# Optimization experiments

Hardware: AMD Instinct MI355X
Metric: run time of the kernel (lower is better)

The kernel has to match this reference:

```python
import jax, jax.numpy as jnp
import numpy as np

TOP_K = 2


def setup_inputs() -> dict:
    key = jax.random.key(0)
    k1, k2, k3, k4, k5 = jax.random.split(key, 5)
    B, S, H, F, E = 4, 2048, 1024, 4096, 8
    scale = 1.0 / np.sqrt(H)
    return {
        "hidden_states": jax.random.normal(k1, (B, S, H), dtype=jnp.float32),
        "gate_w": jax.random.normal(k2, (E, H), dtype=jnp.float32) * scale,
        "w1": jax.random.normal(k3, (E, F, H), dtype=jnp.float32) * scale,
        "w3": jax.random.normal(k4, (E, F, H), dtype=jnp.float32) * scale,
        "w2": jax.random.normal(k5, (E, H, F), dtype=jnp.float32) * (1.0 / np.sqrt(F)),
    }


def reference(hidden_states, gate_w, w1, w3, w2):
    B, S, H = hidden_states.shape
    E = gate_w.shape[0]
    x = hidden_states.reshape(-1, H)                    # [T, H], T = B*S

    router_logits = x @ gate_w.T                        # [T, E]
    probs = jax.nn.softmax(router_logits.astype(jnp.float32), axis=-1)
    top_w, top_i = jax.lax.top_k(probs, TOP_K)          # [T, k]
    top_w = top_w / jnp.sum(top_w, axis=-1, keepdims=True)
    top_w = top_w.astype(x.dtype)

    # combine weight of each expert for each token: [E, T]
    one_hot = jax.nn.one_hot(top_i, E, dtype=x.dtype)   # [T, k, E]
    comb = jnp.einsum("tke,tk->et", one_hot, top_w)

    # loop over experts via scan; tokens not routed to expert e have comb==0,
    # which matches the gather/FFN/scatter-combine of the original exactly.
    def body(acc, wts):
        w1e, w3e, w2e, ce = wts
        h = jax.nn.silu(x @ w1e.T) * (x @ w3e.T)        # [T, F]
        return acc + (h @ w2e.T) * ce[:, None], None

    out0 = jnp.zeros_like(x)
    out, _ = jax.lax.scan(body, out0, (w1, w3, w2, comb))
    return out.reshape(B, S, H), router_logits
```

## Files before the change

### kernel.cpp

```cpp
#include <hip/hip_runtime.h>
#include <hip/hip_bf16.h>

#define T_TOK 8192
#define HDIM  1024
#define FDIM  4096
#define NEXP  8

typedef __attribute__((ext_vector_type(8))) short short8;
typedef __attribute__((ext_vector_type(4))) float f32x4;
typedef unsigned short u16;
typedef unsigned int   u32;

#define XB_OFF    0ull
#define W1B_OFF   (XB_OFF   + 16777216ull)
#define W3B_OFF   (W1B_OFF  + 67108864ull)
#define W2B_OFF   (W3B_OFF  + 67108864ull)
#define HBUF_OFF  (W2B_OFF  + 67108864ull)
#define CNT_OFF   (HBUF_OFF + 134217728ull)
#define HOFF_OFF  (CNT_OFF  + 64ull)
#define TLIST_OFF (HOFF_OFF + 64ull)
#define WLIST_OFF (TLIST_OFF + 262144ull)
#define WS_NEED   (WLIST_OFF + 262144ull)

__device__ __forceinline__ u16 f2bf(float f) {
  u32 u = __float_as_uint(f);
  return (u16)((u + 0x7fffu + ((u >> 16) & 1u)) >> 16);
}

__device__ __forceinline__ void gl_lds16(const void* g, void* l) {
  __builtin_amdgcn_global_load_lds(
      (const __attribute__((address_space(1))) void*)g,
      (__attribute__((address_space(3))) void*)l, 16, 0, 0);
}

__global__ __launch_bounds__(256) void convert_kernel(const float* __restrict__ src,
                                                      u16* __restrict__ dst, int n4) {
  int stride = gridDim.x * blockDim.x;
  for (int i = blockIdx.x * blockDim.x + threadIdx.x; i < n4; i += stride) {
    float4 v = ((const float4*)src)[i];
    u32 lo = (u32)f2bf(v.x) | ((u32)f2bf(v.y) << 16);
    u32 hi = (u32)f2bf(v.z) | ((u32)f2bf(v.w) << 16);
    ((uint2*)dst)[i] = make_uint2(lo, hi);
  }
}

__global__ __launch_bounds__(256) void router_kernel(
    const float* __restrict__ x, const float* __restrict__ gw,
    float* __restrict__ logits, u16* __restrict__ xb,
    int* __restrict__ counts, int* __restrict__ tlist, float* __restrict__ wlist) {
  const int wid = threadIdx.x >> 6, lane = threadIdx.x & 63;
  const int t = blockIdx.x * 4 + wid;
  const float* xr = x + (size_t)t * HDIM + lane * 16;
  float4 xv[4];
#pragma unroll
  for (int q = 0; q < 4; ++q) xv[q] = ((const float4*)xr)[q];

  u32 pk[8];
#pragma unroll
  for (int q = 0; q < 4; ++q) {
    pk[q * 2 + 0] = (u32)f2bf(xv[q].x) | ((u32)f2bf(xv[q].y) << 16);
    pk[q * 2 + 1] = (u32)f2bf(xv[q].z) | ((u32)f2bf(xv[q].w) << 16);
  }
  u32* xbo = (u32*)(xb + (size_t)t * HDIM + lane * 16);
  ((uint4*)xbo)[0] = make_uint4(pk[0], pk[1], pk[2], pk[3]);
  ((uint4*)xbo)[1] = make_uint4(pk[4], pk[5], pk[6], pk[7]);

  float lg[NEXP];
#pragma unroll
  for (int e = 0; e < NEXP; ++e) {
    const float4* g = (const float4*)(gw + (size_t)e * HDIM + lane * 16);
    float s = 0.f;
#pragma unroll
    for (int q = 0; q < 4; ++q) {
      float4 gv = g[q];
      s += xv[q].x * gv.x + xv[q].y * gv.y + xv[q].z * gv.z + xv[q].w * gv.w;
    }
#pragma unroll
    for (int off = 32; off > 0; off >>= 1) s += __shfl_xor(s, off, 64);
    lg[e] = s;
  }
  if (lane == 0) {
    float* lo = logits + (size_t)t * NEXP;
#pragma unroll
    for (int e = 0; e < NEXP; ++e) lo[e] = lg[e];
    float v1 = -1e30f, v2 = -1e30f; int i1 = 0, i2 = 0;
#pragma unroll
    for (int e = 0; e < NEXP; ++e) {
      float le = lg[e];
      if (le > v1)      { v2 = v1; i2 = i1; v1 = le; i1 = e; }
      else if (le > v2) { v2 = le; i2 = e; }
    }
    float t2 = __expf(v2 - v1);
    float rs = 1.f / (1.f + t2);
    int p1 = atomicAdd(&counts[i1], 1);
    tlist[i1 * T_TOK + p1] = t; wlist[i1 * T_TOK + p1] = rs;
    int p2 = atomicAdd(&counts[i2], 1);
    tlist[i2 * T_TOK + p2] = t; wlist[i2 * T_TOK + p2] = t2 * rs;
  }
}

__global__ void prefix_kernel(const int* __restrict__ counts, int* __restrict__ hoff) {
  if (threadIdx.x == 0) {
    int s = 0;
    for (int e = 0; e < NEXP; ++e) { hoff[e] = s; s += counts[e]; }
    hoff[NEXP] = s;
  }
}

__global__ __launch_bounds__(256, 2) void ffn1_kernel(
    const u16* __restrict__ xb, const u16* __restrict__ w1b, const u16* __restrict__ w3b,
    u16* __restrict__ hbuf, const int* __restrict__ counts, const int* __restrict__ hoff,
    const int* __restrict__ tlist) {
  const int bid = blockIdx.x;
  const int e  = bid & 7;
  const int j  = bid >> 3;
  const int ct = j >> 6;
  const int rt = j & 63;
  const int Ne = counts[e];
  if (rt * 128 >= Ne) return;

  __shared__ u16 Alds[128 * 64];
  __shared__ u16 B1lds[128 * 64];
  __shared__ u16 B3lds[128 * 64];

  const int tid = threadIdx.x;
  const int wid = tid >> 6, lane = tid & 63;
  const int wr = wid >> 1, wc = wid & 1;
  const int lr = lane & 15, lhi = lane >> 4;

  size_t aoff[4], boff[4]; int ldso[4];
#pragma unroll
  for (int q = 0; q < 4; ++q) {
    int i = wid * 4 + q;
    int r = i * 8 + (lane >> 3);
    int sw = ((lane & 7) ^ (r & 7)) * 8;
    int grow = rt * 128 + r;
    int gi = grow < Ne ? grow : Ne - 1;
    int tok = tlist[e * T_TOK + gi];
    aoff[q] = (size_t)tok * HDIM + sw;
    int fr = ct * 128 + r;
    boff[q] = ((size_t)e * FDIM + fr) * HDIM + sw;
    ldso[q] = i * 512;
  }

  f32x4 acc1[4][4] = {}; f32x4 acc3[4][4] = {};

  for (int k0 = 0; k0 < HDIM; k0 += 64) {
    __syncthreads();
#pragma unroll
    for (int q = 0; q < 4; ++q) {
      gl_lds16(xb  + aoff[q] + k0, Alds  + ldso[q]);
      gl_lds16(w1b + boff[q] + k0, B1lds + ldso[q]);
      gl_lds16(w3b + boff[q] + k0, B3lds + ldso[q]);
    }
    __syncthreads();
#pragma unroll
    for (int kk = 0; kk < 2; ++kk) {
      const int swo = ((kk * 4 + lhi) ^ (lr & 7)) * 8;
      short8 af[4], b1f[4], b3f[4];
#pragma unroll
      for (int m = 0; m < 4; ++m)
        af[m] = *(const short8*)(Alds + (wr * 64 + m * 16 + lr) * 64 + swo);
#pragma unroll
      for (int n = 0; n < 4; ++n) {
        int o = (wc * 64 + n * 16 + lr) * 64 + swo;
        b1f[n] = *(const short8*)(B1lds + o);
        b3f[n] = *(const short8*)(B3lds + o);
      }
#pragma unroll
      for (int m = 0; m < 4; ++m)
#pragma unroll
        for (int n = 0; n < 4; ++n) {
          acc1[m][n] = __builtin_amdgcn_mfma_f32_16x16x32_bf16(af[m], b1f[n], acc1[m][n], 0, 0, 0);
          acc3[m][n] = __builtin_amdgcn_mfma_f32_16x16x32_bf16(af[m], b3f[n], acc3[m][n], 0, 0, 0);
        }
    }
  }

  const int hb = hoff[e];
  const int rbase = rt * 128 + wr * 64 + lhi * 4;
  const int cbase = ct * 128 + wc * 64 + lr;
#pragma unroll
  for (int m = 0; m < 4; ++m)
#pragma unroll
    for (int i = 0; i < 4; ++i) {
      int grow = rbase + m * 16 + i;
      if (grow < Ne) {
        size_t rowp = (size_t)(hb + grow) * FDIM + cbase;
#pragma unroll
        for (int n = 0; n < 4; ++n) {
          float a1 = acc1[m][n][i], a3 = acc3[m][n][i];
          float hv = (a1 / (1.f + __expf(-a1))) * a3;
          hbuf[rowp + n * 16] = f2bf(hv);
        }
      }
    }
}

__global__ __launch_bounds__(256, 2) void ffn2_kernel(
    const u16* __restrict__ hbuf, const u16* __restrict__ w2b,
    float* __restrict__ out, const int* __restrict__ counts, const int* __restrict__ hoff,
    const int* __restrict__ tlist, const float* __restrict__ wlist) {
  const int bid = blockIdx.x;
  const int e  = bid & 7;
  const int j  = bid >> 3;
  const int ct = j >> 6;
  const int rt = j & 63;
  const int Ne = counts[e];
  if (rt * 128 >= Ne) return;
  const int hb = hoff[e];

  __shared__ u16 Alds[128 * 64];
  __shared__ u16 Blds[128 * 64];

  const int tid = threadIdx.x;
  const int wid = tid >> 6, lane = tid & 63;
  const int wr = wid >> 1, wc = wid & 1;
  const int lr = lane & 15, lhi = lane >> 4;

  size_t aoff[4], boff[4]; int ldso[4];
#pragma unroll
  for (int q = 0; q < 4; ++q) {
    int i = wid * 4 + q;
    int r = i * 8 + (lane >> 3);
    int sw = ((lane & 7) ^ (r & 7)) * 8;
    int grow = rt * 128 + r;
    int gi = grow < Ne ? grow : Ne - 1;
    aoff[q] = (size_t)(hb + gi) * FDIM + sw;
    int hr = ct * 128 + r;
    boff[q] = ((size_t)e * HDIM + hr) * FDIM + sw;
    ldso[q] = i * 512;
  }

  f32x4 acc[4][4] = {};

  for (int k0 = 0; k0 < FDIM; k0 += 64) {
    __syncthreads();
#pragma unroll
    for (int q = 0; q < 4; ++q) {
      gl_lds16(hbuf + aoff[q] + k0, Alds + ldso[q]);
      gl_lds16(w2b + boff[q] + k0, Blds + ldso[q]);
    }
    __syncthreads();
#pragma unroll
    for (int kk = 0; kk < 2; ++kk) {
      const int swo = ((kk * 4 + lhi) ^ (lr & 7)) * 8;
      short8 af[4], bf_[4];
#pragma unroll
      for (int m = 0; m < 4; ++m)
        af[m] = *(const short8*)(Alds + (wr * 64 + m * 16 + lr) * 64 + swo);
#pragma unroll
      for (int n = 0; n < 4; ++n)
        bf_[n] = *(const short8*)(Blds + (wc * 64 + n * 16 + lr) * 64 + swo);
#pragma unroll
      for (int m = 0; m < 4; ++m)
#pragma unroll
        for (int n = 0; n < 4; ++n)
          acc[m][n] = __builtin_amdgcn_mfma_f32_16x16x32_bf16(af[m], bf_[n], acc[m][n], 0, 0, 0);
    }
  }

  const int rb = rt * 128 + wr * 64 + lhi * 4;
  const int cb = ct * 128 + wc * 64 + lr;
#pragma unroll
  for (int m = 0; m < 4; ++m)
#pragma unroll
    for (int i = 0; i < 4; ++i) {
      int grow = rb + m * 16 + i;
      if (grow < Ne) {
        int tok = tlist[e * T_TOK + grow];
        float wt = wlist[e * T_TOK + grow];
        float* op = out + (size_t)tok * HDIM + cb;
#pragma unroll
        for (int n = 0; n < 4; ++n)
          atomicAdd(op + n * 16, wt * acc[m][n][i]);
      }
    }
}

extern "C" void kernel_launch(void* const* d_in, const int* in_sizes, int n_in,
                              void* d_out, int out_size, void* d_ws, size_t ws_size,
                              hipStream_t stream) {
  (void)in_sizes; (void)n_in; (void)out_size;
  if (ws_size < WS_NEED) return;

  const float* x  = (const float*)d_in[0];
  const float* gw = (const float*)d_in[1];
  const float* w1 = (const float*)d_in[2];
  const float* w3 = (const float*)d_in[3];
  const float* w2 = (const float*)d_in[4];
  float* out = (float*)d_out;
  float* logits = out + (size_t)T_TOK * HDIM;

  char* ws = (char*)d_ws;
  u16* xb    = (u16*)(ws + XB_OFF);
  u16* w1b   = (u16*)(ws + W1B_OFF);
  u16* w3b   = (u16*)(ws + W3B_OFF);
  u16* w2b   = (u16*)(ws + W2B_OFF);
  u16* hbuf  = (u16*)(ws + HBUF_OFF);
  int* counts = (int*)(ws + CNT_OFF);
  int* hoffp  = (int*)(ws + HOFF_OFF);
  int* tlist  = (int*)(ws + TLIST_OFF);
  float* wlist = (float*)(ws + WLIST_OFF);

  hipMemsetAsync(d_out, 0, (size_t)T_TOK * HDIM * sizeof(float), stream);
  hipMemsetAsync(counts, 0, NEXP * sizeof(int), stream);

  const int n4 = NEXP * FDIM * HDIM / 4;
  convert_kernel<<<4096, 256, 0, stream>>>(w1, w1b, n4);
  convert_kernel<<<4096, 256, 0, stream>>>(w3, w3b, n4);
  convert_kernel<<<4096, 256, 0, stream>>>(w2, w2b, n4);
  router_kernel<<<T_TOK / 4, 256, 0, stream>>>(x, gw, logits, xb, counts, tlist, wlist);
  prefix_kernel<<<1, 64, 0, stream>>>(counts, hoffp);
  ffn1_kernel<<<NEXP * 64 * 32, 256, 0, stream>>>(xb, w1b, w3b, hbuf, counts, hoffp, tlist);
  ffn2_kernel<<<NEXP * 64 * 8, 256, 0, stream>>>(hbuf, w2b, out, counts, hoffp, tlist, wlist);
}
```

Before: 865.7 us.

## Enlarge MoE GEMM tiles to 256 rows, prefetch next K-stage, fuse weight conversions

New measurement: 989.2 us. 14.3% more time.

```diff
diff --git a/kernel.cpp b/kernel.cpp
--- a/kernel.cpp
+++ b/kernel.cpp
@@ -33,14 +33,21 @@
       (__attribute__((address_space(3))) void*)l, 16, 0, 0);
 }
 
-__global__ __launch_bounds__(256) void convert_kernel(const float* __restrict__ src,
-                                                      u16* __restrict__ dst, int n4) {
+__global__ __launch_bounds__(256) void convert3_kernel(
+    const float* __restrict__ s0, const float* __restrict__ s1, const float* __restrict__ s2,
+    u16* __restrict__ d0, u16* __restrict__ d1, u16* __restrict__ d2) {
+  const int n4 = NEXP * FDIM * HDIM / 4;
+  const int total = 3 * n4;
   int stride = gridDim.x * blockDim.x;
-  for (int i = blockIdx.x * blockDim.x + threadIdx.x; i < n4; i += stride) {
-    float4 v = ((const float4*)src)[i];
+  for (int i = blockIdx.x * blockDim.x + threadIdx.x; i < total; i += stride) {
+    int seg = i >> 23;
+    int j = i & (n4 - 1);
+    const float* s = seg == 0 ? s0 : (seg == 1 ? s1 : s2);
+    u16* d = seg == 0 ? d0 : (seg == 1 ? d1 : d2);
+    float4 v = ((const float4*)s)[j];
     u32 lo = (u32)f2bf(v.x) | ((u32)f2bf(v.y) << 16);
     u32 hi = (u32)f2bf(v.z) | ((u32)f2bf(v.w) << 16);
-    ((uint2*)dst)[i] = make_uint2(lo, hi);
+    ((uint2*)d)[j] = make_uint2(lo, hi);
   }
 }
 
@@ -107,19 +114,19 @@
   }
 }
 
-__global__ __launch_bounds__(256, 2) void ffn1_kernel(
+__global__ __launch_bounds__(512, 1) void ffn1_kernel(
     const u16* __restrict__ xb, const u16* __restrict__ w1b, const u16* __restrict__ w3b,
     u16* __restrict__ hbuf, const int* __restrict__ counts, const int* __restrict__ hoff,
     const int* __restrict__ tlist) {
   const int bid = blockIdx.x;
   const int e  = bid & 7;
   const int j  = bid >> 3;
-  const int ct = j >> 6;
-  const int rt = j & 63;
+  const int ct = j >> 5;
+  const int rt = j & 31;
   const int Ne = counts[e];
-  if (rt * 128 >= Ne) return;
-
-  __shared__ u16 Alds[128 * 64];
+  if (rt * 256 >= Ne) return;
+
+  __shared__ u16 Alds[256 * 64];
   __shared__ u16 B1lds[128 * 64];
   __shared__ u16 B3lds[128 * 64];
 
@@ -128,57 +135,69 @@
   const int wr = wid >> 1, wc = wid & 1;
   const int lr = lane & 15, lhi = lane >> 4;
 
-  size_t aoff[4], boff[4]; int ldso[4];
-#pragma unroll
-  for (int q = 0; q < 4; ++q) {
-    int i = wid * 4 + q;
-    int r = i * 8 + (lane >> 3);
-    int sw = ((lane & 7) ^ (r & 7)) * 8;
-    int grow = rt * 128 + r;
+  const int swcol = ((lane & 7) ^ ((lane >> 3) & 7)) * 8;
+  const int rowl  = tid >> 3;
+
+  size_t aoff[4]; int ldsoA[4];
+#pragma unroll
+  for (int i = 0; i < 4; ++i) {
+    int grow = rt * 256 + i * 64 + rowl;
     int gi = grow < Ne ? grow : Ne - 1;
     int tok = tlist[e * T_TOK + gi];
-    aoff[q] = (size_t)tok * HDIM + sw;
-    int fr = ct * 128 + r;
-    boff[q] = ((size_t)e * FDIM + fr) * HDIM + sw;
-    ldso[q] = i * 512;
-  }
+    aoff[i] = (size_t)tok * HDIM + swcol;
+    ldsoA[i] = (i * 64 + wid * 8) * 64;
+  }
+  size_t b1off[2], b3off[2]; int ldsoB[2];
+#pragma unroll
+  for (int i = 0; i < 2; ++i) {
+    int fr = ct * 128 + i * 64 + rowl;
+    b1off[i] = ((size_t)e * FDIM + fr) * HDIM + swcol;
+    b3off[i] = b1off[i];
+    ldsoB[i] = (i * 64 + wid * 8) * 64;
+  }
+
+#define FFN1_STAGE(K0) do { \
+  _Pragma("unroll") for (int i_ = 0; i_ < 4; ++i_) gl_lds16(xb  + aoff[i_]  + (K0), Alds  + ldsoA[i_]); \
+  _Pragma("unroll") for (int i_ = 0; i_ < 2; ++i_) gl_lds16(w1b + b1off[i_] + (K0), B1lds + ldsoB[i_]); \
+  _Pragma("unroll") for (int i_ = 0; i_ < 2; ++i_) gl_lds16(w3b + b3off[i_] + (K0), B3lds + ldsoB[i_]); \
+} while (0)
 
   f32x4 acc1[4][4] = {}; f32x4 acc3[4][4] = {};
+  FFN1_STAGE(0);
 
   for (int k0 = 0; k0 < HDIM; k0 += 64) {
     __syncthreads();
-#pragma unroll
-    for (int q = 0; q < 4; ++q) {
-      gl_lds16(xb  + aoff[q] + k0, Alds  + ldso[q]);
-      gl_lds16(w1b + boff[q] + k0, B1lds + ldso[q]);
-      gl_lds16(w3b + boff[q] + k0, B3lds + ldso[q]);
-    }
-    __syncthreads();
+    short8 af[2][4], b1f[2][4], b3f[2][4];
 #pragma unroll
     for (int kk = 0; kk < 2; ++kk) {
       const int swo = ((kk * 4 + lhi) ^ (lr & 7)) * 8;
-      short8 af[4], b1f[4], b3f[4];
 #pragma unroll
       for (int m = 0; m < 4; ++m)
-        af[m] = *(const short8*)(Alds + (wr * 64 + m * 16 + lr) * 64 + swo);
+        af[kk][m] = *(const short8*)(Alds + (wr * 64 + m * 16 + lr) * 64 + swo);
 #pragma unroll
       for (int n = 0; n < 4; ++n) {
         int o = (wc * 64 + n * 16 + lr) * 64 + swo;
-        b1f[n] = *(const short8*)(B1lds + o);
-        b3f[n] = *(const short8*)(B3lds + o);
+        b1f[kk][n] = *(const short8*)(B1lds + o);
+        b3f[kk][n] = *(const short8*)(B3lds + o);
       }
+    }
+    __syncthreads();
+    if (k0 + 64 < HDIM) FFN1_STAGE(k0 + 64);
+    __builtin_amdgcn_s_setprio(1);
+#pragma unroll
+    for (int kk = 0; kk < 2; ++kk)
 #pragma unroll
       for (int m = 0; m < 4; ++m)
 #pragma unroll
         for (int n = 0; n < 4; ++n) {
-          acc1[m][n] = __builtin_amdgcn_mfma_f32_16x16x32_bf16(af[m], b1f[n], acc1[m][n], 0, 0, 0);
-          acc3[m][n] = __builtin_amdgcn_mfma_f32_16x16x32_bf16(af[m], b3f[n], acc3[m][n], 0, 0, 0);
+          acc1[m][n] = __builtin_amdgcn_mfma_f32_16x16x32_bf16(af[kk][m], b1f[kk][n], acc1[m][n], 0, 0, 0);
+          acc3[m][n] = __builtin_amdgcn_mfma_f32_16x16x32_bf16(af[kk][m], b3f[kk][n], acc3[m][n], 0, 0, 0);
         }
-    }
+    __builtin_amdgcn_s_setprio(0);
   }
 
   const int hb = hoff[e];
-  const int rbase = rt * 128 + wr * 64 + lhi * 4;
+  const int rbase = rt * 256 + wr * 64 + lhi * 4;
   const int cbase = ct * 128 + wc * 64 + lr;
 #pragma unroll
   for (int m = 0; m < 4; ++m)
@@ -195,22 +214,23 @@
         }
       }
     }
-}
-
-__global__ __launch_bounds__(256, 2) void ffn2_kernel(
+#undef FFN1_STAGE
+}
+
+__global__ __launch_bounds__(512, 1) void ffn2_kernel(
     const u16* __restrict__ hbuf, const u16* __restrict__ w2b,
     float* __restrict__ out, const int* __restrict__ counts, const int* __restrict__ hoff,
     const int* __restrict__ tlist, const float* __restrict__ wlist) {
   const int bid = blockIdx.x;
   const int e  = bid & 7;
   const int j  = bid >> 3;
-  const int ct = j >> 6;
-  const int rt = j & 63;
+  const int ct = j >> 5;
+  const int rt = j & 31;
   const int Ne = counts[e];
-  if (rt * 128 >= Ne) return;
+  if (rt * 256 >= Ne) return;
   const int hb = hoff[e];
 
-  __shared__ u16 Alds[128 * 64];
+  __shared__ u16 Alds[256 * 64];
   __shared__ u16 Blds[128 * 64];
 
   const int tid = threadIdx.x;
@@ -218,49 +238,60 @@
   const int wr = wid >> 1, wc = wid & 1;
   const int lr = lane & 15, lhi = lane >> 4;
 
-  size_t aoff[4], boff[4]; int ldso[4];
-#pragma unroll
-  for (int q = 0; q < 4; ++q) {
-    int i = wid * 4 + q;
-    int r = i * 8 + (lane >> 3);
-    int sw = ((lane & 7) ^ (r & 7)) * 8;
-    int grow = rt * 128 + r;
+  const int swcol = ((lane & 7) ^ ((lane >> 3) & 7)) * 8;
+  const int rowl  = tid >> 3;
+
+  size_t aoff[4]; int ldsoA[4];
+#pragma unroll
+  for (int i = 0; i < 4; ++i) {
+    int grow = rt * 256 + i * 64 + rowl;
     int gi = grow < Ne ? grow : Ne - 1;
-    aoff[q] = (size_t)(hb + gi) * FDIM + sw;
-    int hr = ct * 128 + r;
-    boff[q] = ((size_t)e * HDIM + hr) * FDIM + sw;
-    ldso[q] = i * 512;
-  }
+    aoff[i] = (size_t)(hb + gi) * FDIM + swcol;
+    ldsoA[i] = (i * 64 + wid * 8) * 64;
+  }
+  size_t boff[2]; int ldsoB[2];
+#pragma unroll
+  for (int i = 0; i < 2; ++i) {
+    int hr = ct * 128 + i * 64 + rowl;
+    boff[i] = ((size_t)e * HDIM + hr) * FDIM + swcol;
+    ldsoB[i] = (i * 64 + wid * 8) * 64;
+  }
+
+#define FFN2_STAGE(K0) do { \
+  _Pragma("unroll") for (int i_ = 0; i_ < 4; ++i_) gl_lds16(hbuf + aoff[i_] + (K0), Alds + ldsoA[i_]); \
+  _Pragma("unroll") for (int i_ = 0; i_ < 2; ++i_) gl_lds16(w2b  + boff[i_] + (K0), Blds + ldsoB[i_]); \
+} while (0)
 
   f32x4 acc[4][4] = {};
+  FFN2_STAGE(0);
 
   for (int k0 = 0; k0 < FDIM; k0 += 64) {
     __syncthreads();
-#pragma unroll
-    for (int q = 0; q < 4; ++q) {
-      gl_lds16(hbuf + aoff[q] + k0, Alds + ldso[q]);
-      gl_lds16(w2b + boff[q] + k0, Blds + ldso[q]);
-    }
-    __syncthreads();
+    short8 af[2][4], bf_[2][4];
 #pragma unroll
     for (int kk = 0; kk < 2; ++kk) {
       const int swo = ((kk * 4 + lhi) ^ (lr & 7)) * 8;
-      short8 af[4], bf_[4];
 #pragma unroll
       for (int m = 0; m < 4; ++m)
-        af[m] = *(const short8*)(Alds + (wr * 64 + m * 16 + lr) * 64 + swo);
+        af[kk][m] = *(const short8*)(Alds + (wr * 64 + m * 16 + lr) * 64 + swo);
 #pragma unroll
       for (int n = 0; n < 4; ++n)
-        bf_[n] = *(const short8*)(Blds + (wc * 64 + n * 16 + lr) * 64 + swo);
+        bf_[kk][n] = *(const short8*)(Blds + (wc * 64 + n * 16 + lr) * 64 + swo);
+    }
+    __syncthreads();
+    if (k0 + 64 < FDIM) FFN2_STAGE(k0 + 64);
+    __builtin_amdgcn_s_setprio(1);
+#pragma unroll
+    for (int kk = 0; kk < 2; ++kk)
 #pragma unroll
       for (int m = 0; m < 4; ++m)
 #pragma unroll
         for (int n = 0; n < 4; ++n)
-          acc[m][n] = __builtin_amdgcn_mfma_f32_16x16x32_bf16(af[m], bf_[n], acc[m][n], 0, 0, 0);
-    }
-  }
-
-  const int rb = rt * 128 + wr * 64 + lhi * 4;
+          acc[m][n] = __builtin_amdgcn_mfma_f32_16x16x32_bf16(af[kk][m], bf_[kk][n], acc[m][n], 0, 0, 0);
+    __builtin_amdgcn_s_setprio(0);
+  }
+
+  const int rb = rt * 256 + wr * 64 + lhi * 4;
   const int cb = ct * 128 + wc * 64 + lr;
 #pragma unroll
   for (int m = 0; m < 4; ++m)
@@ -276,6 +307,7 @@
           atomicAdd(op + n * 16, wt * acc[m][n][i]);
       }
     }
+#undef FFN2_STAGE
 }
 
 extern "C" void kernel_launch(void* const* d_in, const int* in_sizes, int n_in,
@@ -306,12 +338,9 @@
   hipMemsetAsync(d_out, 0, (size_t)T_TOK * HDIM * sizeof(float), stream);
   hipMemsetAsync(counts, 0, NEXP * sizeof(int), stream);
 
-  const int n4 = NEXP * FDIM * HDIM / 4;
-  convert_kernel<<<4096, 256, 0, stream>>>(w1, w1b, n4);
-  convert_kernel<<<4096, 256, 0, stream>>>(w3, w3b, n4);
-  convert_kernel<<<4096, 256, 0, stream>>>(w2, w2b, n4);
+  convert3_kernel<<<8192, 256, 0, stream>>>(w1, w3, w2, w1b, w3b, w2b);
   router_kernel<<<T_TOK / 4, 256, 0, stream>>>(x, gw, logits, xb, counts, tlist, wlist);
   prefix_kernel<<<1, 64, 0, stream>>>(counts, hoffp);
-  ffn1_kernel<<<NEXP * 64 * 32, 256, 0, stream>>>(xb, w1b, w3b, hbuf, counts, hoffp, tlist);
-  ffn2_kernel<<<NEXP * 64 * 8, 256, 0, stream>>>(hbuf, w2b, out, counts, hoffp, tlist, wlist);
-}
+  ffn1_kernel<<<NEXP * 32 * 32, 512, 0, stream>>>(xb, w1b, w3b, hbuf, counts, hoffp, tlist);
+  ffn2_kernel<<<NEXP * 8 * 32, 512, 0, stream>>>(hbuf, w2b, out, counts, hoffp, tlist, wlist);
+}
```

## Fuse weight conversion with router and use 8-wave ffn1 blocks

Applied to the files above, without the earlier changes.

Measured after the change: 833.2 us. -3.8%, faster.

```diff
diff --git a/kernel.cpp b/kernel.cpp
--- a/kernel.cpp
+++ b/kernel.cpp
@@ -33,23 +33,34 @@
       (__attribute__((address_space(3))) void*)l, 16, 0, 0);
 }
 
-__global__ __launch_bounds__(256) void convert_kernel(const float* __restrict__ src,
-                                                      u16* __restrict__ dst, int n4) {
-  int stride = gridDim.x * blockDim.x;
-  for (int i = blockIdx.x * blockDim.x + threadIdx.x; i < n4; i += stride) {
-    float4 v = ((const float4*)src)[i];
-    u32 lo = (u32)f2bf(v.x) | ((u32)f2bf(v.y) << 16);
-    u32 hi = (u32)f2bf(v.z) | ((u32)f2bf(v.w) << 16);
-    ((uint2*)dst)[i] = make_uint2(lo, hi);
-  }
-}
-
-__global__ __launch_bounds__(256) void router_kernel(
+__global__ __launch_bounds__(256) void prep_kernel(
     const float* __restrict__ x, const float* __restrict__ gw,
+    const float* __restrict__ s0, const float* __restrict__ s1, const float* __restrict__ s2,
+    u16* __restrict__ d0, u16* __restrict__ d1, u16* __restrict__ d2,
     float* __restrict__ logits, u16* __restrict__ xb,
     int* __restrict__ counts, int* __restrict__ tlist, float* __restrict__ wlist) {
+  if (blockIdx.x < 8192) {
+    const int n8 = NEXP * FDIM * HDIM / 8;
+    const int total = 3 * n8;
+    const int stride = 8192 * 256;
+    for (int i = blockIdx.x * 256 + threadIdx.x; i < total; i += stride) {
+      int seg = i >> 22;
+      int j = i & (n8 - 1);
+      const float* s = seg == 0 ? s0 : (seg == 1 ? s1 : s2);
+      u16* d = seg == 0 ? d0 : (seg == 1 ? d1 : d2);
+      float4 v0 = ((const float4*)s)[j * 2];
+      float4 v1 = ((const float4*)s)[j * 2 + 1];
+      uint4 o;
+      o.x = (u32)f2bf(v0.x) | ((u32)f2bf(v0.y) << 16);
+      o.y = (u32)f2bf(v0.z) | ((u32)f2bf(v0.w) << 16);
+      o.z = (u32)f2bf(v1.x) | ((u32)f2bf(v1.y) << 16);
+      o.w = (u32)f2bf(v1.z) | ((u32)f2bf(v1.w) << 16);
+      ((uint4*)d)[j] = o;
+    }
+    return;
+  }
   const int wid = threadIdx.x >> 6, lane = threadIdx.x & 63;
-  const int t = blockIdx.x * 4 + wid;
+  const int t = (blockIdx.x - 8192) * 4 + wid;
   const float* xr = x + (size_t)t * HDIM + lane * 16;
   float4 xv[4];
 #pragma unroll
@@ -107,7 +118,7 @@
   }
 }
 
-__global__ __launch_bounds__(256, 2) void ffn1_kernel(
+__global__ __launch_bounds__(512, 2) void ffn1_kernel(
     const u16* __restrict__ xb, const u16* __restrict__ w1b, const u16* __restrict__ w3b,
     u16* __restrict__ hbuf, const int* __restrict__ counts, const int* __restrict__ hoff,
     const int* __restrict__ tlist) {
@@ -119,58 +130,56 @@
   const int Ne = counts[e];
   if (rt * 128 >= Ne) return;
 
-  __shared__ u16 Alds[128 * 64];
-  __shared__ u16 B1lds[128 * 64];
-  __shared__ u16 B3lds[128 * 64];
+  __shared__ u16 LDS[24576];
 
   const int tid = threadIdx.x;
   const int wid = tid >> 6, lane = tid & 63;
-  const int wr = wid >> 1, wc = wid & 1;
+  const int wr = wid >> 2, wc = wid & 3;
   const int lr = lane & 15, lhi = lane >> 4;
 
-  size_t aoff[4], boff[4]; int ldso[4];
-#pragma unroll
-  for (int q = 0; q < 4; ++q) {
-    int i = wid * 4 + q;
-    int r = i * 8 + (lane >> 3);
-    int sw = ((lane & 7) ^ (r & 7)) * 8;
+  size_t aoff[2], b1off[2], b3off[2];
+#pragma unroll
+  for (int q = 0; q < 2; ++q) {
+    int idx = q * 512 + tid;
+    int r = idx >> 3, c = idx & 7;
+    int sw = (c ^ (r & 7)) * 8;
     int grow = rt * 128 + r;
     int gi = grow < Ne ? grow : Ne - 1;
-    int tok = tlist[e * T_TOK + gi];
-    aoff[q] = (size_t)tok * HDIM + sw;
+    aoff[q]  = (size_t)tlist[e * T_TOK + gi] * HDIM + sw;
     int fr = ct * 128 + r;
-    boff[q] = ((size_t)e * FDIM + fr) * HDIM + sw;
-    ldso[q] = i * 512;
-  }
-
-  f32x4 acc1[4][4] = {}; f32x4 acc3[4][4] = {};
+    b1off[q] = ((size_t)e * FDIM + fr) * HDIM + sw;
+    b3off[q] = b1off[q];
+  }
+  const int dW = wid * 512;
+
+  f32x4 acc1[4][2] = {}, acc3[4][2] = {};
 
   for (int k0 = 0; k0 < HDIM; k0 += 64) {
     __syncthreads();
 #pragma unroll
-    for (int q = 0; q < 4; ++q) {
-      gl_lds16(xb  + aoff[q] + k0, Alds  + ldso[q]);
-      gl_lds16(w1b + boff[q] + k0, B1lds + ldso[q]);
-      gl_lds16(w3b + boff[q] + k0, B3lds + ldso[q]);
+    for (int q = 0; q < 2; ++q) {
+      gl_lds16(xb  + aoff[q]  + k0, LDS + q * 4096 + dW);
+      gl_lds16(w1b + b1off[q] + k0, LDS + 8192 + q * 4096 + dW);
+      gl_lds16(w3b + b3off[q] + k0, LDS + 16384 + q * 4096 + dW);
     }
     __syncthreads();
 #pragma unroll
     for (int kk = 0; kk < 2; ++kk) {
-      const int swo = ((kk * 4 + lhi) ^ (lr & 7)) * 8;
-      short8 af[4], b1f[4], b3f[4];
+      const int chn = ((kk * 4 + lhi) ^ (lr & 7)) * 8;
+      short8 af[4], b1f[2], b3f[2];
 #pragma unroll
       for (int m = 0; m < 4; ++m)
-        af[m] = *(const short8*)(Alds + (wr * 64 + m * 16 + lr) * 64 + swo);
-#pragma unroll
-      for (int n = 0; n < 4; ++n) {
-        int o = (wc * 64 + n * 16 + lr) * 64 + swo;
-        b1f[n] = *(const short8*)(B1lds + o);
-        b3f[n] = *(const short8*)(B3lds + o);
+        af[m] = *(const short8*)(LDS + (wr * 64 + m * 16 + lr) * 64 + chn);
+#pragma unroll
+      for (int n = 0; n < 2; ++n) {
+        int ro = (wc * 32 + n * 16 + lr) * 64 + chn;
+        b1f[n] = *(const short8*)(LDS + 8192 + ro);
+        b3f[n] = *(const short8*)(LDS + 16384 + ro);
       }
 #pragma unroll
       for (int m = 0; m < 4; ++m)
 #pragma unroll
-        for (int n = 0; n < 4; ++n) {
+        for (int n = 0; n < 2; ++n) {
           acc1[m][n] = __builtin_amdgcn_mfma_f32_16x16x32_bf16(af[m], b1f[n], acc1[m][n], 0, 0, 0);
           acc3[m][n] = __builtin_amdgcn_mfma_f32_16x16x32_bf16(af[m], b3f[n], acc3[m][n], 0, 0, 0);
         }
@@ -179,7 +188,7 @@
 
   const int hb = hoff[e];
   const int rbase = rt * 128 + wr * 64 + lhi * 4;
-  const int cbase = ct * 128 + wc * 64 + lr;
+  const int cbase = ct * 128 + wc * 32 + lr;
 #pragma unroll
   for (int m = 0; m < 4; ++m)
 #pragma unroll
@@ -188,10 +197,9 @@
       if (grow < Ne) {
         size_t rowp = (size_t)(hb + grow) * FDIM + cbase;
 #pragma unroll
-        for (int n = 0; n < 4; ++n) {
+        for (int n = 0; n < 2; ++n) {
           float a1 = acc1[m][n][i], a3 = acc3[m][n][i];
-          float hv = (a1 / (1.f + __expf(-a1))) * a3;
-          hbuf[rowp + n * 16] = f2bf(hv);
+          hbuf[rowp + n * 16] = f2bf((a1 / (1.f + __expf(-a1))) * a3);
         }
       }
     }
@@ -306,12 +314,9 @@
   hipMemsetAsync(d_out, 0, (size_t)T_TOK * HDIM * sizeof(float), stream);
   hipMemsetAsync(counts, 0, NEXP * sizeof(int), stream);
 
-  const int n4 = NEXP * FDIM * HDIM / 4;
-  convert_kernel<<<4096, 256, 0, stream>>>(w1, w1b, n4);
-  convert_kernel<<<4096, 256, 0, stream>>>(w3, w3b, n4);
-  convert_kernel<<<4096, 256, 0, stream>>>(w2, w2b, n4);
-  router_kernel<<<T_TOK / 4, 256, 0, stream>>>(x, gw, logits, xb, counts, tlist, wlist);
+  prep_kernel<<<8192 + 2048, 256, 0, stream>>>(x, gw, w1, w3, w2, w1b, w3b, w2b,
+                                               logits, xb, counts, tlist, wlist);
   prefix_kernel<<<1, 64, 0, stream>>>(counts, hoffp);
-  ffn1_kernel<<<NEXP * 64 * 32, 256, 0, stream>>>(xb, w1b, w3b, hbuf, counts, hoffp, tlist);
+  ffn1_kernel<<<NEXP * 64 * 32, 512, 0, stream>>>(xb, w1b, w3b, hbuf, counts, hoffp, tlist);
   ffn2_kernel<<<NEXP * 64 * 8, 256, 0, stream>>>(hbuf, w2b, out, counts, hoffp, tlist, wlist);
 }
```
